# Performance work log

Hardware: AMD Instinct MI355X
Metric: run time of the kernel (lower is better)

Reference implementation:

```python
import jax, jax.numpy as jnp
import numpy as np

B, T, L, D = 2, 16, 256, 1152
NH, HD = 16, 72
MLP_H = int(int(D * 4.0) * 2 / 3)  # 3072, per SwiGLUFFN


def _rms(x, w, eps=1e-6):
    return x * jax.lax.rsqrt(jnp.mean(jnp.square(x), axis=-1, keepdims=True) + eps) * w


def _attn(x, qkv_w, qkv_b, qn, kn, proj_w, proj_b, nh):
    Bn, N, C = x.shape
    hd = C // nh
    qkv = (x @ qkv_w + qkv_b).reshape(Bn, N, 3, nh, hd)
    qkv = jnp.transpose(qkv, (2, 0, 3, 1, 4))  # [3, Bn, nh, N, hd]
    q, k, v = qkv[0], qkv[1], qkv[2]
    q = _rms(q, qn)
    k = _rms(k, kn)
    scores = jnp.einsum('bhnd,bhmd->bhnm', q, k) / jnp.sqrt(jnp.float32(hd))
    a = jax.nn.softmax(scores, axis=-1)
    o = jnp.einsum('bhnm,bhmd->bhnd', a, v)
    o = jnp.transpose(o, (0, 2, 1, 3)).reshape(Bn, N, C)
    return o @ proj_w + proj_b


def setup_inputs() -> dict:
    key = jax.random.key(0)
    ks = jax.random.split(key, 12)
    w = lambda k, shape: jax.random.normal(k, shape, jnp.float32) * 0.02
    return {
        'x': jax.random.normal(ks[0], (B, T, L, D), jnp.float32),
        'c': jax.random.normal(ks[1], (B, D), jnp.float32),
        'norm1_w': jnp.ones((D,), jnp.float32),
        'norm2_w': jnp.ones((D,), jnp.float32),
        'norm3_w': jnp.ones((D,), jnp.float32),
        'qn_s': jnp.ones((HD,), jnp.float32),
        'kn_s': jnp.ones((HD,), jnp.float32),
        'qkv_s_w': w(ks[2], (D, 3 * D)),
        'qkv_s_b': jnp.zeros((3 * D,), jnp.float32),
        'proj_s_w': w(ks[3], (D, D)),
        'proj_s_b': jnp.zeros((D,), jnp.float32),
        'qn_t': jnp.ones((HD,), jnp.float32),
        'kn_t': jnp.ones((HD,), jnp.float32),
        'qkv_t_w': w(ks[4], (D, 3 * D)),
        'qkv_t_b': jnp.zeros((3 * D,), jnp.float32),
        'proj_t_w': w(ks[5], (D, D)),
        'proj_t_b': jnp.zeros((D,), jnp.float32),
        'w12_w': w(ks[6], (D, 2 * MLP_H)),
        'w12_b': jnp.zeros((2 * MLP_H,), jnp.float32),
        'w3_w': w(ks[7], (MLP_H, D)),
        'w3_b': jnp.zeros((D,), jnp.float32),
        'ada_w': w(ks[8], (D, 9 * D)),
        'ada_b': jnp.zeros((9 * D,), jnp.float32),
    }


def reference(x, c, norm1_w, norm2_w, norm3_w,
              qn_s, kn_s, qkv_s_w, qkv_s_b, proj_s_w, proj_s_b,
              qn_t, kn_t, qkv_t_w, qkv_t_b, proj_t_w, proj_t_b,
              w12_w, w12_b, w3_w, w3_b, ada_w, ada_b):
    Bb, Tt, Ll, Dd = x.shape
    # adaLN_modulation: SiLU then Linear, chunk into 9 [B, D] tensors
    ch = (jax.nn.silu(c) @ ada_w + ada_b).reshape(Bb, 9, Dd)
    sh_s, sc_s, g_s = ch[:, 0], ch[:, 1], ch[:, 2]
    sh_t, sc_t, g_t = ch[:, 3], ch[:, 4], ch[:, 5]
    sh_m, sc_m, g_m = ch[:, 6], ch[:, 7], ch[:, 8]

    # spatial attention over L, folded batch B*T
    x_s = x.reshape(Bb * Tt, Ll, Dd)
    shs = jnp.repeat(sh_s, Tt, axis=0)[:, None, :]   # [B*T,1,D]
    scs = jnp.repeat(sc_s, Tt, axis=0)[:, None, :]
    gs = jnp.repeat(g_s, Tt, axis=0)[:, None, :]
    xn = _rms(x_s, norm1_w) * (1 + scs) + shs
    x_s = x_s + gs * _attn(xn, qkv_s_w, qkv_s_b, qn_s, kn_s, proj_s_w, proj_s_b, NH)
    x = x_s.reshape(Bb, Tt, Ll, Dd)

    # temporal attention over T, folded batch B*L
    x_t = jnp.transpose(x, (0, 2, 1, 3)).reshape(Bb * Ll, Tt, Dd)
    sht = jnp.repeat(sh_t, Ll, axis=0)[:, None, :]
    sct = jnp.repeat(sc_t, Ll, axis=0)[:, None, :]
    gt = jnp.repeat(g_t, Ll, axis=0)[:, None, :]
    xn = _rms(x_t, norm2_w) * (1 + sct) + sht
    x_t = x_t + gt * _attn(xn, qkv_t_w, qkv_t_b, qn_t, kn_t, proj_t_w, proj_t_b, NH)
    x = jnp.transpose(x_t.reshape(Bb, Ll, Tt, Dd), (0, 2, 1, 3))

    # SwiGLU MLP with adaLN modulate + gate
    xn = _rms(x, norm3_w) * (1 + sc_m[:, None, None, :]) + sh_m[:, None, None, :]
    x12 = xn @ w12_w + w12_b
    x1, x2 = jnp.split(x12, 2, axis=-1)
    mlp_out = (jax.nn.silu(x1) * x2) @ w3_w + w3_b
    x = x + g_m[:, None, None, :] * mlp_out
    return x
```

## Files before the change

### kernel.cpp

```cpp
#include <hip/hip_runtime.h>
#include <stdint.h>

typedef __bf16 bf16x8 __attribute__((ext_vector_type(8)));
typedef float f32x4 __attribute__((ext_vector_type(4)));

__device__ __forceinline__ float b2f(uint32_t u) {
  union { uint32_t i; float f; } v; v.i = u << 16; return v.f;
}
__device__ __forceinline__ uint16_t f2b(float f) {
  union { float f; uint32_t i; } v; v.f = f;
  uint32_t r = (v.i + 0x7fffu + ((v.i >> 16) & 1u)) >> 16;
  return (uint16_t)r;
}
__device__ __forceinline__ void unpack8(uint4 u, float* f) {
  f[0] = b2f(u.x & 0xffffu); f[1] = b2f(u.x >> 16);
  f[2] = b2f(u.y & 0xffffu); f[3] = b2f(u.y >> 16);
  f[4] = b2f(u.z & 0xffffu); f[5] = b2f(u.z >> 16);
  f[6] = b2f(u.w & 0xffffu); f[7] = b2f(u.w >> 16);
}

__device__ __forceinline__ void gl2lds16(const void* g, void* l) {
  __builtin_amdgcn_global_load_lds(
      (const __attribute__((address_space(1))) void*)g,
      (__attribute__((address_space(3))) void*)l, 16, 0, 0);
}

__global__ __launch_bounds__(256) void gemm_k(
    const uint16_t* __restrict__ A, const uint16_t* __restrict__ Bt,
    const float* __restrict__ bias,
    uint16_t* __restrict__ outb,
    float* __restrict__ outf, const float* __restrict__ resid,
    const float* __restrict__ gate,
    int N, int K, int mode)
{
  __shared__ __align__(16) uint16_t As[2][128 * 32];
  __shared__ __align__(16) uint16_t Bs[2][128 * 32];
  const int tid = threadIdx.x;
  const int xcd = blockIdx.x & 7;
  const int slot = blockIdx.x >> 3;
  const int mt = xcd * 8 + (slot & 7);
  const int nt = slot >> 3;
  const int row0 = mt * 128, col0 = nt * 128;

  const int lane = tid & 63, wave = tid >> 6;
  const int l15 = lane & 15, quad = lane >> 4;
  const int wm = (wave & 1) * 64, wn = (wave >> 1) * 64;

  f32x4 acc[4][4];
  const f32x4 zero = {0.f, 0.f, 0.f, 0.f};
  for (int i = 0; i < 4; i++)
    for (int j = 0; j < 4; j++)
      acc[i][j] = zero;

  const int rseg = wave * 32 + (lane >> 2);
  const int kseg8 = (lane & 3) * 8;
  const uint16_t* gA = A + (size_t)(row0 + rseg) * K + kseg8;
  const uint16_t* gB = Bt + (size_t)(col0 + rseg) * K + kseg8;
  const size_t rowK16 = (size_t)16 * K;
  const int woff = wave * 2048;

  gl2lds16(gA,          (char*)As[0] + woff);
  gl2lds16(gA + rowK16, (char*)As[0] + woff + 1024);
  gl2lds16(gB,          (char*)Bs[0] + woff);
  gl2lds16(gB + rowK16, (char*)Bs[0] + woff + 1024);

  for (int k0 = 0; k0 < K; k0 += 32) {
    const int cur = (k0 >> 5) & 1;
    __syncthreads();
    if (k0 + 32 < K) {
      const int nxt = cur ^ 1;
      gl2lds16(gA + k0 + 32,          (char*)As[nxt] + woff);
      gl2lds16(gA + rowK16 + k0 + 32, (char*)As[nxt] + woff + 1024);
      gl2lds16(gB + k0 + 32,          (char*)Bs[nxt] + woff);
      gl2lds16(gB + rowK16 + k0 + 32, (char*)Bs[nxt] + woff + 1024);
    }

    bf16x8 af[4], bfr[4];
#pragma unroll
    for (int i = 0; i < 4; i++) {
      af[i]  = *(const bf16x8*)&As[cur][(wm + i * 16 + l15) * 32 + quad * 8];
      bfr[i] = *(const bf16x8*)&Bs[cur][(wn + i * 16 + l15) * 32 + quad * 8];
    }
#pragma unroll
    for (int mi = 0; mi < 4; mi++)
#pragma unroll
      for (int ni = 0; ni < 4; ni++)
        acc[mi][ni] = __builtin_amdgcn_mfma_f32_16x16x32_bf16(af[mi], bfr[ni], acc[mi][ni], 0, 0, 0);
  }

#pragma unroll
  for (int mi = 0; mi < 4; mi++) {
#pragma unroll
    for (int ni = 0; ni < 4; ni++) {
      const int colg = col0 + wn + ni * 16 + l15;
      const float bv = bias ? bias[colg] : 0.f;
#pragma unroll
      for (int i = 0; i < 4; i++) {
        const int rowg = row0 + wm + mi * 16 + quad * 4 + i;
        const float v = acc[mi][ni][i] + bv;
        const size_t idx = (size_t)rowg * N + colg;
        if (mode == 0) {
          outb[idx] = f2b(v);
        } else {
          const int b = rowg >> 12;
          outf[idx] = resid[idx] + gate[b * 10368 + colg] * v;
        }
      }
    }
  }
}

__global__ __launch_bounds__(256) void rmsnorm_k(
    const float* __restrict__ x, const float* __restrict__ w,
    const float* __restrict__ chv, int shsel, int scsel,
    uint16_t* __restrict__ xn)
{
  const int row = blockIdx.x;
  const int b = row >> 12;
  const float* xr = x + (size_t)row * 1152;
  float ss = 0.f;
  for (int d = threadIdx.x; d < 1152; d += 256) { const float v = xr[d]; ss += v * v; }
  for (int off = 32; off > 0; off >>= 1) ss += __shfl_down(ss, off);
  __shared__ float red[4];
  if ((threadIdx.x & 63) == 0) red[threadIdx.x >> 6] = ss;
  __syncthreads();
  const float tot = red[0] + red[1] + red[2] + red[3];
  const float rs = rsqrtf(tot * (1.f / 1152.f) + 1e-6f);
  const float* sh = chv + b * 10368 + shsel * 1152;
  const float* sc = chv + b * 10368 + scsel * 1152;
  uint16_t* xo = xn + (size_t)row * 1152;
  for (int d = threadIdx.x; d < 1152; d += 256)
    xo[d] = f2b(xr[d] * rs * w[d] * (1.f + sc[d]) + sh[d]);
}

__global__ __launch_bounds__(256) void qknorm_k(
    uint16_t* __restrict__ qkv, const float* __restrict__ qn, const float* __restrict__ kn)
{
  const int tid = threadIdx.x;
  const int rl = tid >> 5, unit = tid & 31;
  const int h = unit & 15, isK = unit >> 4;
  const size_t row = (size_t)blockIdx.x * 8 + rl;
  uint16_t* p = qkv + row * 3456 + isK * 1152 + h * 72;
  const float* w = isK ? kn : qn;
  float v[72];
#pragma unroll
  for (int i = 0; i < 9; i++) unpack8(((const uint4*)p)[i], v + i * 8);
  float ss = 0.f;
#pragma unroll
  for (int d = 0; d < 72; d++) ss += v[d] * v[d];
  const float rs = rsqrtf(ss * (1.f / 72.f) + 1e-6f);
#pragma unroll
  for (int d = 0; d < 72; d++) p[d] = f2b(v[d] * rs * w[d]);
}

#define AK_STRIDE 104
#define VT_STRIDE 88
#define PS_STRIDE 72
__global__ __launch_bounds__(256) void attn_s_k(
    const uint16_t* __restrict__ qkv, uint16_t* __restrict__ out)
{
  __shared__ __align__(16) uint16_t Ks[64 * AK_STRIDE];
  __shared__ __align__(16) uint16_t Vt[80 * VT_STRIDE];
  __shared__ __align__(16) uint16_t Ps[4 * 64 * PS_STRIDE];
  const int bh = blockIdx.x;
  const int bt = bh >> 4, h = bh & 15;
  const int tid = threadIdx.x;
  const int lane = tid & 63, wave = tid >> 6;
  const int l15 = lane & 15, quad = lane >> 4;
  const size_t rowbase = (size_t)bt * 256;
  const float scale = 0.1178511301977579f;

  union { uint4 u; bf16x8 v; } zu; zu.u = make_uint4(0, 0, 0, 0);
  const bf16x8 zero8 = zu.v;

  bf16x8 qf[4][3];
#pragma unroll
  for (int mi = 0; mi < 4; mi++) {
    const uint16_t* qp = qkv + (rowbase + wave * 64 + mi * 16 + l15) * 3456 + h * 72;
    qf[mi][0] = *(const bf16x8*)(qp + quad * 8);
    qf[mi][1] = *(const bf16x8*)(qp + 32 + quad * 8);
    qf[mi][2] = (quad == 0) ? *(const bf16x8*)(qp + 64) : zero8;
  }

  f32x4 oacc[4][5];
#pragma unroll
  for (int mi = 0; mi < 4; mi++)
#pragma unroll
    for (int dt = 0; dt < 5; dt++)
      oacc[mi][dt] = (f32x4){0.f, 0.f, 0.f, 0.f};
  float mrun[4][4], lrun[4][4];
#pragma unroll
  for (int mi = 0; mi < 4; mi++)
#pragma unroll
    for (int i = 0; i < 4; i++) { mrun[mi][i] = -1e30f; lrun[mi][i] = 0.f; }

  uint16_t* psw = &Ps[wave * 64 * PS_STRIDE];

  for (int c = 0; c < 4; c++) {
    __syncthreads();
    for (int idx = tid; idx < 576; idx += 256) {
      const int rr = idx / 9, cc = idx - rr * 9;
      const uint16_t* kg = qkv + (rowbase + c * 64 + rr) * 3456 + 1152 + h * 72 + cc * 8;
      *(uint4*)&Ks[rr * AK_STRIDE + cc * 8] = *(const uint4*)kg;
      uint4 vv = *(const uint4*)(kg + 1152);
      const uint16_t* e = (const uint16_t*)&vv;
#pragma unroll
      for (int j = 0; j < 8; j++) Vt[(cc * 8 + j) * VT_STRIDE + rr] = e[j];
    }
    __syncthreads();

    f32x4 s[4][4];
#pragma unroll
    for (int mi = 0; mi < 4; mi++)
#pragma unroll
      for (int ni = 0; ni < 4; ni++)
        s[mi][ni] = (f32x4){0.f, 0.f, 0.f, 0.f};
#pragma unroll
    for (int ni = 0; ni < 4; ni++) {
      bf16x8 kf0 = *(const bf16x8*)&Ks[(ni * 16 + l15) * AK_STRIDE + quad * 8];
      bf16x8 kf1 = *(const bf16x8*)&Ks[(ni * 16 + l15) * AK_STRIDE + 32 + quad * 8];
      bf16x8 kf2 = (quad == 0) ? *(const bf16x8*)&Ks[(ni * 16 + l15) * AK_STRIDE + 64] : zero8;
#pragma unroll
      for (int mi = 0; mi < 4; mi++) {
        s[mi][ni] = __builtin_amdgcn_mfma_f32_16x16x32_bf16(qf[mi][0], kf0, s[mi][ni], 0, 0, 0);
        s[mi][ni] = __builtin_amdgcn_mfma_f32_16x16x32_bf16(qf[mi][1], kf1, s[mi][ni], 0, 0, 0);
        s[mi][ni] = __builtin_amdgcn_mfma_f32_16x16x32_bf16(qf[mi][2], kf2, s[mi][ni], 0, 0, 0);
      }
    }

#pragma unroll
    for (int mi = 0; mi < 4; mi++) {
#pragma unroll
      for (int i = 0; i < 4; i++) {
        float mx = fmaxf(fmaxf(s[mi][0][i], s[mi][1][i]), fmaxf(s[mi][2][i], s[mi][3][i])) * scale;
#pragma unroll
        for (int d = 1; d < 16; d <<= 1) mx = fmaxf(mx, __shfl_xor(mx, d));
        const float mnew = fmaxf(mrun[mi][i], mx);
        const float corr = __expf(mrun[mi][i] - mnew);
        mrun[mi][i] = mnew;
        float psum = 0.f;
#pragma unroll
        for (int ni = 0; ni < 4; ni++) {
          const float p = __expf(s[mi][ni][i] * scale - mnew);
          s[mi][ni][i] = p;
          psum += p;
        }
#pragma unroll
        for (int d = 1; d < 16; d <<= 1) psum += __shfl_xor(psum, d);
        lrun[mi][i] = lrun[mi][i] * corr + psum;
#pragma unroll
        for (int dt = 0; dt < 5; dt++) oacc[mi][dt][i] *= corr;
      }
    }

#pragma unroll
    for (int mi = 0; mi < 4; mi++)
#pragma unroll
      for (int ni = 0; ni < 4; ni++)
#pragma unroll
        for (int i = 0; i < 4; i++)
          psw[(mi * 16 + quad * 4 + i) * PS_STRIDE + ni * 16 + l15] = f2b(s[mi][ni][i]);

#pragma unroll
    for (int kk = 0; kk < 2; kk++) {
      bf16x8 pf[4];
#pragma unroll
      for (int mi = 0; mi < 4; mi++)
        pf[mi] = *(const bf16x8*)&psw[(mi * 16 + l15) * PS_STRIDE + kk * 32 + quad * 8];
#pragma unroll
      for (int dt = 0; dt < 5; dt++) {
        bf16x8 vf = *(const bf16x8*)&Vt[(dt * 16 + l15) * VT_STRIDE + kk * 32 + quad * 8];
#pragma unroll
        for (int mi = 0; mi < 4; mi++)
          oacc[mi][dt] = __builtin_amdgcn_mfma_f32_16x16x32_bf16(pf[mi], vf, oacc[mi][dt], 0, 0, 0);
      }
    }
  }

#pragma unroll
  for (int mi = 0; mi < 4; mi++) {
#pragma unroll
    for (int i = 0; i < 4; i++) {
      const float inv = 1.f / lrun[mi][i];
      const size_t orow = rowbase + wave * 64 + mi * 16 + quad * 4 + i;
#pragma unroll
      for (int dt = 0; dt < 5; dt++) {
        const int d = dt * 16 + l15;
        if (d < 72) out[orow * 1152 + h * 72 + d] = f2b(oacc[mi][dt][i] * inv);
      }
    }
  }
}

__global__ __launch_bounds__(128) void attn_t_k(
    const uint16_t* __restrict__ qkv, uint16_t* __restrict__ out)
{
  const int blk = blockIdx.x;
  const int bl = blk >> 1, hg = blk & 1;
  const int b = bl >> 8, l = bl & 255;
  const int tid = threadIdx.x;
  const int hh = tid >> 4, tq = tid & 15;
  const int h = hg * 8 + hh;
  __shared__ __align__(16) uint16_t kb[8 * 16 * 72];
  __shared__ __align__(16) uint16_t vb[8 * 16 * 72];

#pragma unroll
  for (int it = 0; it < 9; it++) {
    const int idx = tid + it * 128;
    const int rowL = idx / 9, cc = idx % 9;
    const int hhL = rowL >> 4, tL = rowL & 15;
    const size_t grow = (size_t)b * 4096 + (size_t)tL * 256 + l;
    const int colk = 1152 + (hg * 8 + hhL) * 72 + cc * 8;
    ((uint4*)&kb[rowL * 72])[cc] = *(const uint4*)(qkv + grow * 3456 + colk);
    ((uint4*)&vb[rowL * 72])[cc] = *(const uint4*)(qkv + grow * 3456 + colk + 1152);
  }
  __syncthreads();

  float q[72];
  const size_t qrow = (size_t)b * 4096 + (size_t)tq * 256 + l;
  {
    const uint16_t* qp = qkv + qrow * 3456 + h * 72;
#pragma unroll
    for (int i = 0; i < 9; i++) unpack8(((const uint4*)qp)[i], q + i * 8);
  }
  const float scale = 0.1178511301977579f;
  float s[16];
#pragma unroll
  for (int m = 0; m < 16; m++) {
    const uint4* kr = (const uint4*)&kb[(hh * 16 + m) * 72];
    float a = 0.f;
#pragma unroll
    for (int i = 0; i < 9; i++) {
      float kf[8]; unpack8(kr[i], kf);
#pragma unroll
      for (int j = 0; j < 8; j++) a += q[i * 8 + j] * kf[j];
    }
    s[m] = a * scale;
  }
  float mx = -1e30f;
#pragma unroll
  for (int m = 0; m < 16; m++) mx = fmaxf(mx, s[m]);
  float sum = 0.f;
#pragma unroll
  for (int m = 0; m < 16; m++) { s[m] = __expf(s[m] - mx); sum += s[m]; }
  const float inv = 1.f / sum;
  float o[72];
#pragma unroll
  for (int d = 0; d < 72; d++) o[d] = 0.f;
#pragma unroll
  for (int m = 0; m < 16; m++) {
    const float p = s[m];
    const uint4* vr = (const uint4*)&vb[(hh * 16 + m) * 72];
#pragma unroll
    for (int i = 0; i < 9; i++) {
      float vf[8]; unpack8(vr[i], vf);
#pragma unroll
      for (int j = 0; j < 8; j++) o[i * 8 + j] += p * vf[j];
    }
  }
  uint16_t* op = out + qrow * 1152 + h * 72;
#pragma unroll
  for (int d = 0; d < 72; d++) op[d] = f2b(o[d] * inv);
}

__global__ __launch_bounds__(256) void transcvt_k(
    const float* __restrict__ in, uint16_t* __restrict__ out, int K, int N)
{
  __shared__ float t[32][33];
  const int n0 = blockIdx.x * 32, k0 = blockIdx.y * 32;
  const int tx = threadIdx.x & 31, ty = threadIdx.x >> 5;
#pragma unroll
  for (int i = 0; i < 32; i += 8)
    t[ty + i][tx] = in[(size_t)(k0 + ty + i) * N + n0 + tx];
  __syncthreads();
#pragma unroll
  for (int i = 0; i < 32; i += 8)
    out[(size_t)(n0 + ty + i) * K + k0 + tx] = f2b(t[tx][ty + i]);
}

__global__ __launch_bounds__(256) void swiglu_k(
    const uint16_t* __restrict__ x1, const uint16_t* __restrict__ x2, uint16_t* __restrict__ h)
{
  const size_t i = ((size_t)blockIdx.x * 256 + threadIdx.x) * 8;
  float a[8], bb[8];
  unpack8(*(const uint4*)(x1 + i), a);
  unpack8(*(const uint4*)(x2 + i), bb);
  uint32_t r[4];
#pragma unroll
  for (int j = 0; j < 4; j++) {
    const float s0 = a[2 * j]     / (1.f + __expf(-a[2 * j]))     * bb[2 * j];
    const float s1 = a[2 * j + 1] / (1.f + __expf(-a[2 * j + 1])) * bb[2 * j + 1];
    r[j] = (uint32_t)f2b(s0) | ((uint32_t)f2b(s1) << 16);
  }
  *(uint4*)(h + i) = make_uint4(r[0], r[1], r[2], r[3]);
}

__global__ void siluc_k(const float* __restrict__ c, float* __restrict__ cs) {
  const int i = blockIdx.x * 256 + threadIdx.x;
  if (i < 2304) { const float v = c[i]; cs[i] = v / (1.f + __expf(-v)); }
}

#define ADA_KS 18
#define ADA_RK 64
__global__ __launch_bounds__(256) void ada_part_k(
    const float* __restrict__ cs, const float* __restrict__ W,
    float* __restrict__ part)
{
  const int col = blockIdx.x * 256 + threadIdx.x;
  const int ks = blockIdx.y;
  const int k0 = ks * ADA_RK;
  __shared__ float sc0[ADA_RK], sc1[ADA_RK];
  if (threadIdx.x < ADA_RK) sc0[threadIdx.x] = cs[k0 + threadIdx.x];
  else if (threadIdx.x < 2 * ADA_RK) sc1[threadIdx.x - ADA_RK] = cs[1152 + k0 + threadIdx.x - ADA_RK];
  __syncthreads();
  if (col >= 10368) return;
  const float* Wp = W + (size_t)k0 * 10368 + col;
  float s0 = 0.f, s1 = 0.f;
#pragma unroll 8
  for (int r = 0; r < ADA_RK; r++) {
    const float wv = Wp[(size_t)r * 10368];
    s0 += sc0[r] * wv;
    s1 += sc1[r] * wv;
  }
  part[(size_t)(ks * 2 + 0) * 10368 + col] = s0;
  part[(size_t)(ks * 2 + 1) * 10368 + col] = s1;
}

__global__ __launch_bounds__(256) void ada_reduce_k(
    const float* __restrict__ part, const float* __restrict__ bias,
    float* __restrict__ chv)
{
  const int col = blockIdx.x * 256 + threadIdx.x;
  if (col >= 10368) return;
  float s0 = bias[col], s1 = bias[col];
#pragma unroll
  for (int ks = 0; ks < ADA_KS; ks++) {
    s0 += part[(size_t)(ks * 2 + 0) * 10368 + col];
    s1 += part[(size_t)(ks * 2 + 1) * 10368 + col];
  }
  chv[col] = s0;
  chv[10368 + col] = s1;
}

extern "C" void kernel_launch(void* const* d_in, const int* in_sizes, int n_in,
                              void* d_out, int out_size, void* d_ws, size_t ws_size,
                              hipStream_t stream)
{
  const float* c_in    = (const float*)d_in[1];
  const float* norm1w  = (const float*)d_in[2];
  const float* norm2w  = (const float*)d_in[3];
  const float* norm3w  = (const float*)d_in[4];
  const float* qn_s    = (const float*)d_in[5];
  const float* kn_s    = (const float*)d_in[6];
  const float* qkv_s_w = (const float*)d_in[7];
  const float* qkv_s_b = (const float*)d_in[8];
  const float* proj_s_w= (const float*)d_in[9];
  const float* proj_s_b= (const float*)d_in[10];
  const float* qn_t    = (const float*)d_in[11];
  const float* kn_t    = (const float*)d_in[12];
  const float* qkv_t_w = (const float*)d_in[13];
  const float* qkv_t_b = (const float*)d_in[14];
  const float* proj_t_w= (const float*)d_in[15];
  const float* proj_t_b= (const float*)d_in[16];
  const float* w12_w   = (const float*)d_in[17];
  const float* w12_b   = (const float*)d_in[18];
  const float* w3_w    = (const float*)d_in[19];
  const float* w3_b    = (const float*)d_in[20];
  const float* ada_w   = (const float*)d_in[21];
  const float* ada_b   = (const float*)d_in[22];

  float* X = (float*)d_out;

  char* wsb = (char*)d_ws; size_t off = 0;
  auto alloc = [&](size_t bytes) -> void* {
    void* p = wsb + off; off += bytes; off = (off + 255) & ~(size_t)255; return p;
  };
  uint16_t* XN    = (uint16_t*)alloc((size_t)8192 * 1152 * 2);
  uint16_t* QKV   = (uint16_t*)alloc((size_t)8192 * 3456 * 2);
  uint16_t* X2    = (uint16_t*)alloc((size_t)8192 * 3072 * 2);
  uint16_t* WqkvS = (uint16_t*)alloc((size_t)3456 * 1152 * 2);
  uint16_t* WprojS= (uint16_t*)alloc((size_t)1152 * 1152 * 2);
  uint16_t* WqkvT = (uint16_t*)alloc((size_t)3456 * 1152 * 2);
  uint16_t* WprojT= (uint16_t*)alloc((size_t)1152 * 1152 * 2);
  uint16_t* W12T  = (uint16_t*)alloc((size_t)6144 * 1152 * 2);
  uint16_t* W3T   = (uint16_t*)alloc((size_t)1152 * 3072 * 2);
  float* CH = (float*)alloc((size_t)2 * 10368 * 4);
  float* CS = (float*)alloc((size_t)2 * 1152 * 4);
  float* APART = (float*)alloc((size_t)ADA_KS * 2 * 10368 * 4);

  hipMemcpyAsync(X, d_in[0], (size_t)8192 * 1152 * 4, hipMemcpyDeviceToDevice, stream);
  siluc_k<<<9, 256, 0, stream>>>(c_in, CS);
  ada_part_k<<<dim3(41, ADA_KS), 256, 0, stream>>>(CS, ada_w, APART);
  ada_reduce_k<<<41, 256, 0, stream>>>(APART, ada_b, CH);

  transcvt_k<<<dim3(3456 / 32, 1152 / 32), 256, 0, stream>>>(qkv_s_w, WqkvS, 1152, 3456);
  transcvt_k<<<dim3(1152 / 32, 1152 / 32), 256, 0, stream>>>(proj_s_w, WprojS, 1152, 1152);
  transcvt_k<<<dim3(3456 / 32, 1152 / 32), 256, 0, stream>>>(qkv_t_w, WqkvT, 1152, 3456);
  transcvt_k<<<dim3(1152 / 32, 1152 / 32), 256, 0, stream>>>(proj_t_w, WprojT, 1152, 1152);
  transcvt_k<<<dim3(6144 / 32, 1152 / 32), 256, 0, stream>>>(w12_w, W12T, 1152, 6144);
  transcvt_k<<<dim3(1152 / 32, 3072 / 32), 256, 0, stream>>>(w3_w, W3T, 3072, 1152);

  rmsnorm_k<<<8192, 256, 0, stream>>>(X, norm1w, CH, 0, 1, XN);
  gemm_k<<<27 * 64, 256, 0, stream>>>(XN, WqkvS, qkv_s_b, QKV, nullptr, nullptr, nullptr,
                                      3456, 1152, 0);
  qknorm_k<<<1024, 256, 0, stream>>>(QKV, qn_s, kn_s);
  attn_s_k<<<512, 256, 0, stream>>>(QKV, XN);
  gemm_k<<<9 * 64, 256, 0, stream>>>(XN, WprojS, proj_s_b, nullptr, X, X, CH + 2 * 1152,
                                     1152, 1152, 1);

  rmsnorm_k<<<8192, 256, 0, stream>>>(X, norm2w, CH, 3, 4, XN);
  gemm_k<<<27 * 64, 256, 0, stream>>>(XN, WqkvT, qkv_t_b, QKV, nullptr, nullptr, nullptr,
                                      3456, 1152, 0);
  qknorm_k<<<1024, 256, 0, stream>>>(QKV, qn_t, kn_t);
  attn_t_k<<<1024, 128, 0, stream>>>(QKV, XN);
  gemm_k<<<9 * 64, 256, 0, stream>>>(XN, WprojT, proj_t_b, nullptr, X, X, CH + 5 * 1152,
                                     1152, 1152, 1);

  rmsnorm_k<<<8192, 256, 0, stream>>>(X, norm3w, CH, 6, 7, XN);
  gemm_k<<<24 * 64, 256, 0, stream>>>(XN, W12T, w12_b, QKV, nullptr, nullptr, nullptr,
                                      3072, 1152, 0);
  gemm_k<<<24 * 64, 256, 0, stream>>>(XN, W12T + (size_t)3072 * 1152, w12_b + 3072, X2,
                                      nullptr, nullptr, nullptr, 3072, 1152, 0);
  swiglu_k<<<12288, 256, 0, stream>>>(QKV, X2, QKV);
  gemm_k<<<9 * 64, 256, 0, stream>>>(QKV, W3T, w3_b, nullptr, X, X, CH + 8 * 1152,
                                     1152, 3072, 1);
}
```

Measured before the change: 1.045 ms.

## Replace GEMM with 256x256 tiled, swizzled, phase-pipelined kernel and merge W12 GEMMs

Replaces the 128x128 GEMM with a 512-thread, 256x256-tile kernel. It uses XOR-swizzled LDS layouts, K=64 double-buffered stages split into four interleaved load/MFMA phases, explicit waitcnt and barriers, and s_setprio around the MFMA blocks. The two W12 GEMMs become one N=6144 GEMM, and swiglu now runs in place on the interleaved output, with an lda parameter so W3 reads the strided half. The larger tile reduces global traffic per FLOP, at the cost of padded tiles (N=3456 and 1152 are not multiples of 256), fewer blocks for the small-N GEMMs, and reads past the valid weight rows, which the enlarged weight allocations must cover.

```diff
diff --git a/kernel.cpp b/kernel.cpp
--- a/kernel.cpp
+++ b/kernel.cpp
@@ -25,85 +25,135 @@
       (__attribute__((address_space(3))) void*)l, 16, 0, 0);
 }
 
-__global__ __launch_bounds__(256) void gemm_k(
-    const uint16_t* __restrict__ A, const uint16_t* __restrict__ Bt,
+__global__ __launch_bounds__(512, 2) void gemm256_k(
+    const uint16_t* __restrict__ A, int lda,
+    const uint16_t* __restrict__ Bt,
     const float* __restrict__ bias,
     uint16_t* __restrict__ outb,
     float* __restrict__ outf, const float* __restrict__ resid,
     const float* __restrict__ gate,
     int N, int K, int mode)
 {
-  __shared__ __align__(16) uint16_t As[2][128 * 32];
-  __shared__ __align__(16) uint16_t Bs[2][128 * 32];
+  __shared__ __align__(16) uint16_t L[65536];
   const int tid = threadIdx.x;
+  const int lane = tid & 63, wave = tid >> 6;
+  const int l15 = lane & 15, quad = lane >> 4;
+  const int wm = (wave >> 2) * 128, wn = (wave & 3) * 64;
+
   const int xcd = blockIdx.x & 7;
   const int slot = blockIdx.x >> 3;
-  const int mt = xcd * 8 + (slot & 7);
-  const int nt = slot >> 3;
-  const int row0 = mt * 128, col0 = nt * 128;
-
-  const int lane = tid & 63, wave = tid >> 6;
-  const int l15 = lane & 15, quad = lane >> 4;
-  const int wm = (wave & 1) * 64, wn = (wave >> 1) * 64;
-
-  f32x4 acc[4][4];
-  const f32x4 zero = {0.f, 0.f, 0.f, 0.f};
-  for (int i = 0; i < 4; i++)
+  const int mt = xcd * 4 + (slot & 3);
+  const int nt = slot >> 2;
+  const int row0 = mt * 256, col0 = nt * 256;
+
+  const int NTk = K >> 6;
+
+  const uint16_t* Ag = A + (size_t)row0 * lda;
+  const uint16_t* Bg = Bt + (size_t)col0 * K;
+
+  const int sX = (lane & 7) ^ (lane >> 3);
+  const int laneRowA = lane >> 3;
+  const int laneK8A = sX * 8;
+  const int laneRowB = 2 * (lane >> 3) + ((sX >> 2) & 1);
+  const int laneK8B = (sX & 3) * 8;
+  const int rA0 = ((wave * 16) & 63) + (((wave * 16) >> 6) << 7);
+  const int rB0 = wave * 32;
+
+#define STAGE_A(BUF, SUB, KT) do { \
+    const uint16_t* g_ = Ag + (size_t)(rA0 + (SUB) * 64 + laneRowA) * lda + (size_t)(KT) * 64 + laneK8A; \
+    uint16_t* l_ = (uint16_t*)&L[(BUF) * 32768 + (rA0 + (SUB) * 64) * 64]; \
+    gl2lds16(g_, l_); \
+    gl2lds16(g_ + (size_t)8 * lda, l_ + 512); \
+  } while (0)
+
+#define STAGE_B(BUF, HALF, KT) do { \
+    const uint16_t* g_ = Bg + (size_t)(rB0 + laneRowB) * K + (size_t)(KT) * 64 + (HALF) * 32 + laneK8B; \
+    uint16_t* l_ = (uint16_t*)&L[(BUF) * 32768 + 16384 + (HALF) * 8192 + rB0 * 32]; \
+    gl2lds16(g_, l_); \
+    gl2lds16(g_ + (size_t)16 * K, l_ + 512); \
+  } while (0)
+
+  f32x4 acc[8][4];
+#pragma unroll
+  for (int i = 0; i < 8; i++)
+#pragma unroll
     for (int j = 0; j < 4; j++)
-      acc[i][j] = zero;
-
-  const int rseg = wave * 32 + (lane >> 2);
-  const int kseg8 = (lane & 3) * 8;
-  const uint16_t* gA = A + (size_t)(row0 + rseg) * K + kseg8;
-  const uint16_t* gB = Bt + (size_t)(col0 + rseg) * K + kseg8;
-  const size_t rowK16 = (size_t)16 * K;
-  const int woff = wave * 2048;
-
-  gl2lds16(gA,          (char*)As[0] + woff);
-  gl2lds16(gA + rowK16, (char*)As[0] + woff + 1024);
-  gl2lds16(gB,          (char*)Bs[0] + woff);
-  gl2lds16(gB + rowK16, (char*)Bs[0] + woff + 1024);
-
-  for (int k0 = 0; k0 < K; k0 += 32) {
-    const int cur = (k0 >> 5) & 1;
-    __syncthreads();
-    if (k0 + 32 < K) {
-      const int nxt = cur ^ 1;
-      gl2lds16(gA + k0 + 32,          (char*)As[nxt] + woff);
-      gl2lds16(gA + rowK16 + k0 + 32, (char*)As[nxt] + woff + 1024);
-      gl2lds16(gB + k0 + 32,          (char*)Bs[nxt] + woff);
-      gl2lds16(gB + rowK16 + k0 + 32, (char*)Bs[nxt] + woff + 1024);
-    }
-
-    bf16x8 af[4], bfr[4];
-#pragma unroll
-    for (int i = 0; i < 4; i++) {
-      af[i]  = *(const bf16x8*)&As[cur][(wm + i * 16 + l15) * 32 + quad * 8];
-      bfr[i] = *(const bf16x8*)&Bs[cur][(wn + i * 16 + l15) * 32 + quad * 8];
-    }
-#pragma unroll
-    for (int mi = 0; mi < 4; mi++)
-#pragma unroll
-      for (int ni = 0; ni < 4; ni++)
-        acc[mi][ni] = __builtin_amdgcn_mfma_f32_16x16x32_bf16(af[mi], bfr[ni], acc[mi][ni], 0, 0, 0);
-  }
-
-#pragma unroll
-  for (int mi = 0; mi < 4; mi++) {
+      acc[i][j] = (f32x4){0.f, 0.f, 0.f, 0.f};
+
+  bf16x8 a_[4], b_[4];
+
+#define PHASE(CUR, KK, QM, READB, STAGE_STMT, VM_STMT) do { \
+    _Pragma("unroll") for (int mi = 0; mi < 4; mi++) \
+      a_[mi] = *(const bf16x8*)&L[(CUR) * 32768 + (wm + (QM) * 64 + mi * 16 + l15) * 64 + \
+                                  ((((KK) * 4 + quad) ^ (l15 & 7)) * 8)]; \
+    if (READB) { \
+      _Pragma("unroll") for (int ni = 0; ni < 4; ni++) \
+        b_[ni] = *(const bf16x8*)&L[(CUR) * 32768 + 16384 + (KK) * 8192 + \
+                                    ((wn >> 1) + ni * 8 + (l15 >> 1)) * 64 + \
+                                    ((((((l15 & 1) << 2) | quad)) ^ (l15 >> 1)) * 8)]; \
+    } \
+    STAGE_STMT; \
+    __builtin_amdgcn_sched_barrier(0); \
+    __builtin_amdgcn_s_barrier(); \
+    asm volatile("s_waitcnt lgkmcnt(0)" ::: "memory"); \
+    __builtin_amdgcn_sched_barrier(0); \
+    __builtin_amdgcn_s_setprio(1); \
+    _Pragma("unroll") for (int mi = 0; mi < 4; mi++) \
+      _Pragma("unroll") for (int ni = 0; ni < 4; ni++) \
+        acc[(QM) * 4 + mi][ni] = __builtin_amdgcn_mfma_f32_16x16x32_bf16( \
+            a_[mi], b_[ni], acc[(QM) * 4 + mi][ni], 0, 0, 0); \
+    __builtin_amdgcn_s_setprio(0); \
+    __builtin_amdgcn_sched_barrier(0); \
+    VM_STMT; \
+    __builtin_amdgcn_sched_barrier(0); \
+    __builtin_amdgcn_s_barrier(); \
+    __builtin_amdgcn_sched_barrier(0); \
+  } while (0)
+
+#define TILE(CUR, T) do { \
+    PHASE(CUR, 0, 0, 1, { if ((T) + 1 < NTk) STAGE_B((CUR) ^ 1, 1, (T) + 1); }, {}); \
+    PHASE(CUR, 0, 1, 0, { if ((T) + 1 < NTk) STAGE_A((CUR) ^ 1, 1, (T) + 1); }, {}); \
+    PHASE(CUR, 1, 0, 1, { if ((T) + 2 < NTk) STAGE_B((CUR), 0, (T) + 2); }, {}); \
+    PHASE(CUR, 1, 1, 0, { if ((T) + 2 < NTk) STAGE_A((CUR), 0, (T) + 2); }, \
+      { if ((T) + 2 < NTk) { asm volatile("s_waitcnt vmcnt(4)" ::: "memory"); } \
+        else               { asm volatile("s_waitcnt vmcnt(0)" ::: "memory"); } }); \
+  } while (0)
+
+  STAGE_A(0, 0, 0); STAGE_A(0, 1, 0); STAGE_B(0, 0, 0); STAGE_B(0, 1, 0);
+  STAGE_A(1, 0, 1); STAGE_B(1, 0, 1);
+  asm volatile("s_waitcnt vmcnt(4)" ::: "memory");
+  __builtin_amdgcn_sched_barrier(0);
+  __builtin_amdgcn_s_barrier();
+  __builtin_amdgcn_sched_barrier(0);
+
+  for (int t = 0; t < NTk; t += 2) {
+    TILE(0, t);
+    TILE(1, t + 1);
+  }
+
+#undef PHASE
+#undef TILE
+#undef STAGE_A
+#undef STAGE_B
+
+#pragma unroll
+  for (int mi = 0; mi < 8; mi++) {
 #pragma unroll
     for (int ni = 0; ni < 4; ni++) {
       const int colg = col0 + wn + ni * 16 + l15;
-      const float bv = bias ? bias[colg] : 0.f;
-#pragma unroll
-      for (int i = 0; i < 4; i++) {
-        const int rowg = row0 + wm + mi * 16 + quad * 4 + i;
-        const float v = acc[mi][ni][i] + bv;
-        const size_t idx = (size_t)rowg * N + colg;
-        if (mode == 0) {
-          outb[idx] = f2b(v);
-        } else {
-          const int b = rowg >> 12;
-          outf[idx] = resid[idx] + gate[b * 10368 + colg] * v;
+      if (colg < N) {
+        const float bv = bias ? bias[colg] : 0.f;
+#pragma unroll
+        for (int i = 0; i < 4; i++) {
+          const int rowg = row0 + wm + mi * 16 + quad * 4 + i;
+          const float v = acc[mi][ni][i] + bv;
+          const size_t idx = (size_t)rowg * N + colg;
+          if (mode == 0) {
+            outb[idx] = f2b(v);
+          } else {
+            const int b = rowg >> 12;
+            outf[idx] = resid[idx] + gate[b * 10368 + colg] * v;
+          }
         }
       }
     }
@@ -378,13 +428,14 @@
     out[(size_t)(n0 + ty + i) * K + k0 + tx] = f2b(t[tx][ty + i]);
 }
 
-__global__ __launch_bounds__(256) void swiglu_k(
-    const uint16_t* __restrict__ x1, const uint16_t* __restrict__ x2, uint16_t* __restrict__ h)
-{
-  const size_t i = ((size_t)blockIdx.x * 256 + threadIdx.x) * 8;
+__global__ __launch_bounds__(256) void swiglu_k(uint16_t* __restrict__ x12)
+{
+  const size_t gid = (size_t)blockIdx.x * 256 + threadIdx.x;
+  const size_t row = gid / 384, c8 = gid - row * 384;
+  uint4* base = (uint4*)(x12 + row * 6144);
   float a[8], bb[8];
-  unpack8(*(const uint4*)(x1 + i), a);
-  unpack8(*(const uint4*)(x2 + i), bb);
+  unpack8(base[c8], a);
+  unpack8(base[384 + c8], bb);
   uint32_t r[4];
 #pragma unroll
   for (int j = 0; j < 4; j++) {
@@ -392,7 +443,7 @@
     const float s1 = a[2 * j + 1] / (1.f + __expf(-a[2 * j + 1])) * bb[2 * j + 1];
     r[j] = (uint32_t)f2b(s0) | ((uint32_t)f2b(s1) << 16);
   }
-  *(uint4*)(h + i) = make_uint4(r[0], r[1], r[2], r[3]);
+  base[c8] = make_uint4(r[0], r[1], r[2], r[3]);
 }
 
 __global__ void siluc_k(const float* __restrict__ c, float* __restrict__ cs) {
@@ -476,14 +527,14 @@
     void* p = wsb + off; off += bytes; off = (off + 255) & ~(size_t)255; return p;
   };
   uint16_t* XN    = (uint16_t*)alloc((size_t)8192 * 1152 * 2);
-  uint16_t* QKV   = (uint16_t*)alloc((size_t)8192 * 3456 * 2);
-  uint16_t* X2    = (uint16_t*)alloc((size_t)8192 * 3072 * 2);
-  uint16_t* WqkvS = (uint16_t*)alloc((size_t)3456 * 1152 * 2);
-  uint16_t* WprojS= (uint16_t*)alloc((size_t)1152 * 1152 * 2);
-  uint16_t* WqkvT = (uint16_t*)alloc((size_t)3456 * 1152 * 2);
-  uint16_t* WprojT= (uint16_t*)alloc((size_t)1152 * 1152 * 2);
+  uint16_t* QKV   = (uint16_t*)alloc((size_t)8192 * 6144 * 2);
+  uint16_t* X12   = QKV;
+  uint16_t* WqkvS = (uint16_t*)alloc((size_t)3584 * 1152 * 2);
+  uint16_t* WprojS= (uint16_t*)alloc((size_t)1280 * 1152 * 2);
+  uint16_t* WqkvT = (uint16_t*)alloc((size_t)3584 * 1152 * 2);
+  uint16_t* WprojT= (uint16_t*)alloc((size_t)1280 * 1152 * 2);
   uint16_t* W12T  = (uint16_t*)alloc((size_t)6144 * 1152 * 2);
-  uint16_t* W3T   = (uint16_t*)alloc((size_t)1152 * 3072 * 2);
+  uint16_t* W3T   = (uint16_t*)alloc((size_t)1280 * 3072 * 2);
   float* CH = (float*)alloc((size_t)2 * 10368 * 4);
   float* CS = (float*)alloc((size_t)2 * 1152 * 4);
   float* APART = (float*)alloc((size_t)ADA_KS * 2 * 10368 * 4);
@@ -501,27 +552,25 @@
   transcvt_k<<<dim3(1152 / 32, 3072 / 32), 256, 0, stream>>>(w3_w, W3T, 3072, 1152);
 
   rmsnorm_k<<<8192, 256, 0, stream>>>(X, norm1w, CH, 0, 1, XN);
-  gemm_k<<<27 * 64, 256, 0, stream>>>(XN, WqkvS, qkv_s_b, QKV, nullptr, nullptr, nullptr,
-                                      3456, 1152, 0);
+  gemm256_k<<<32 * 14, 512, 0, stream>>>(XN, 1152, WqkvS, qkv_s_b, QKV, nullptr, nullptr, nullptr,
+                                         3456, 1152, 0);
   qknorm_k<<<1024, 256, 0, stream>>>(QKV, qn_s, kn_s);
   attn_s_k<<<512, 256, 0, stream>>>(QKV, XN);
-  gemm_k<<<9 * 64, 256, 0, stream>>>(XN, WprojS, proj_s_b, nullptr, X, X, CH + 2 * 1152,
-                                     1152, 1152, 1);
+  gemm256_k<<<32 * 5, 512, 0, stream>>>(XN, 1152, WprojS, proj_s_b, nullptr, X, X, CH + 2 * 1152,
+                                        1152, 1152, 1);
 
   rmsnorm_k<<<8192, 256, 0, stream>>>(X, norm2w, CH, 3, 4, XN);
-  gemm_k<<<27 * 64, 256, 0, stream>>>(XN, WqkvT, qkv_t_b, QKV, nullptr, nullptr, nullptr,
-                                      3456, 1152, 0);
+  gemm256_k<<<32 * 14, 512, 0, stream>>>(XN, 1152, WqkvT, qkv_t_b, QKV, nullptr, nullptr, nullptr,
+                                         3456, 1152, 0);
   qknorm_k<<<1024, 256, 0, stream>>>(QKV, qn_t, kn_t);
   attn_t_k<<<1024, 128, 0, stream>>>(QKV, XN);
-  gemm_k<<<9 * 64, 256, 0, stream>>>(XN, WprojT, proj_t_b, nullptr, X, X, CH + 5 * 1152,
-                                     1152, 1152, 1);
+  gemm256_k<<<32 * 5, 512, 0, stream>>>(XN, 1152, WprojT, proj_t_b, nullptr, X, X, CH + 5 * 1152,
+                                        1152, 1152, 1);
 
   rmsnorm_k<<<8192, 256, 0, stream>>>(X, norm3w, CH, 6, 7, XN);
-  gemm_k<<<24 * 64, 256, 0, stream>>>(XN, W12T, w12_b, QKV, nullptr, nullptr, nullptr,
-                                      3072, 1152, 0);
-  gemm_k<<<24 * 64, 256, 0, stream>>>(XN, W12T + (size_t)3072 * 1152, w12_b + 3072, X2,
-                                      nullptr, nullptr, nullptr, 3072, 1152, 0);
-  swiglu_k<<<12288, 256, 0, stream>>>(QKV, X2, QKV);
-  gemm_k<<<9 * 64, 256, 0, stream>>>(QKV, W3T, w3_b, nullptr, X, X, CH + 8 * 1152,
-                                     1152, 3072, 1);
-}
+  gemm256_k<<<32 * 24, 512, 0, stream>>>(XN, 1152, W12T, w12_b, X12, nullptr, nullptr, nullptr,
+                                         6144, 1152, 0);
+  swiglu_k<<<12288, 256, 0, stream>>>(X12);
+  gemm256_k<<<32 * 5, 512, 0, stream>>>(X12, 6144, W3T, w3_b, nullptr, X, X, CH + 8 * 1152,
+                                        1152, 3072, 1);
+}
```

Result: slower. 1.078 ms (+3.2%).
